# Performance work log

Hardware: AMD Instinct MI355X
Metric: run time of the kernel (lower is better)

The kernel has to match this reference:

```python
import jax, jax.numpy as jnp
import numpy as np

NUM_HEADS = 4
K_RATIO = 0.01
K_NEIGHBORS = 8
DIM = 256


def setup_inputs() -> dict:
    key = jax.random.key(0)
    ks = jax.random.split(key, 11)
    d, nh = DIM, NUM_HEADS
    def lin(k, out_f, in_f):
        return jax.random.normal(k, (out_f, in_f), jnp.float32) / np.sqrt(in_f)
    return {
        "x": jax.random.normal(ks[0], (32, d, 64, 64), jnp.float32),
        # graph_modulator: Conv2d(d, d//4, 1) -> ReLU -> Conv2d(d//4, nh, 1) -> Sigmoid
        "gm_w1": lin(ks[1], d // 4, d),
        "gm_b1": jnp.zeros((d // 4,), jnp.float32),
        "gm_w2": lin(ks[2], nh, d // 4),
        "gm_b2": jnp.zeros((nh,), jnp.float32),
        # local_qkv: Linear(d, 3d, bias=False)
        "qkv_w": lin(ks[3], 3 * d, d),
        # graph_encoder: Linear(d, d//2) -> ReLU -> Linear(d//2, nh)
        "ge_w1": lin(ks[4], d // 2, d),
        "ge_b1": jnp.zeros((d // 2,), jnp.float32),
        "ge_w2": lin(ks[5], nh, d // 2),
        "ge_b2": jnp.zeros((nh,), jnp.float32),
    }


def _forward(x, gm_w1, gm_b1, gm_w2, gm_b2, qkv_w, ge_w1, ge_b1, ge_w2, ge_b2):
    B, C, H, W = x.shape
    nh = NUM_HEADS
    hd = C // nh
    scale = hd ** -0.5
    HW = H * W

    # spatial modulation: two 1x1 convs
    h1 = jax.nn.relu(jnp.einsum("bchw,oc->bohw", x, gm_w1) + gm_b1[None, :, None, None])
    spatial_mod = jax.nn.sigmoid(jnp.einsum("bchw,oc->bohw", h1, gm_w2) + gm_b2[None, :, None, None])  # [B,nh,H,W]

    # top-k pixel selection by mean-abs importance
    num_select = min(max(1, int(HW * K_RATIO)), 64)  # static
    importance = jnp.mean(jnp.abs(x), axis=1).reshape(B, HW)
    _, top_idx = jax.lax.top_k(importance, num_select)  # [B,S]

    x_flat = x.reshape(B, C, HW).transpose(0, 2, 1)  # [B,HW,C]
    sel = jnp.take_along_axis(x_flat, top_idx[:, :, None], axis=1)  # [B,S,C]

    def per_batch(feat):  # feat: [S,C]
        S = feat.shape[0]
        # kNN graph on L2-normalized features (F.normalize eps=1e-12)
        n = jnp.maximum(jnp.linalg.norm(feat, axis=1, keepdims=True), 1e-12)
        nf = feat / n
        sim = nf @ nf.T  # [S,S]
        _, nbr = jax.lax.top_k(sim, K_NEIGHBORS + 1)  # [S,k+1]
        rows = jnp.arange(S)[:, None]
        mask = jnp.zeros((S, S), feat.dtype).at[rows, nbr].set(1.0)
        mask = mask * (1.0 - jnp.eye(S, dtype=feat.dtype))  # no self-loops
        # qkv
        qkv = (feat @ qkv_w.T).reshape(S, 3, nh, hd).transpose(1, 2, 0, 3)  # [3,nh,S,hd]
        q, k, v = qkv[0], qkv[1], qkv[2]
        scores = jnp.einsum("hsd,htd->hst", q, k) * scale  # [nh,S,S]
        # graph modulation (same for every head in the torch loop)
        gw = jax.nn.relu(feat @ ge_w1.T + ge_b1) @ ge_w2.T + ge_b2  # [S,nh]
        pair = (gw @ gw.T) / nh  # mean over heads of gw_src*gw_dst
        scores = scores + 0.1 * (mask * pair)[None]
        attn = jax.nn.softmax(scores, axis=-1)
        return attn.mean(axis=(0, 2))  # [S] pixel importance

    pixel_imp = jax.vmap(per_batch)(sel)  # [B,S]

    gmw_flat = jnp.zeros((B, HW), x.dtype).at[jnp.arange(B)[:, None], top_idx].set(pixel_imp)
    graph_mod = jnp.broadcast_to(gmw_flat.reshape(B, 1, H, W), (B, nh, H, W))

    final_mod = 0.7 * spatial_mod + 0.3 * graph_mod
    return x * jnp.mean(final_mod, axis=1, keepdims=True)


def reference(x, gm_w1, gm_b1, gm_w2, gm_b2, qkv_w, ge_w1, ge_b1, ge_w2, ge_b2):
    return _forward(x, gm_w1, gm_b1, gm_w2, gm_b2, qkv_w, ge_w1, ge_b1, ge_w2, ge_b2)
```

## Files before the change

kernel.cpp:

```cpp
#include <hip/hip_runtime.h>
#include <cfloat>

#define B_    32
#define C_    256
#define HW_   4096
#define NH_   4
#define HID_  64
#define SSEL_ 40
#define GADD_ 0.0075f

__global__ __launch_bounds__(256) void k_mlp(
    const float* __restrict__ x,
    const float* __restrict__ w1, const float* __restrict__ b1,
    const float* __restrict__ w2, const float* __restrict__ b2,
    float* __restrict__ m, float* __restrict__ imp)
{
    __shared__ float XT[32 * 128];
    __shared__ float WT[32 * 64];
    __shared__ float H1[64 * 128];
    __shared__ float SAB[256 * 4];

    const int t  = threadIdx.x;
    const int b  = blockIdx.x >> 5;
    const int p0 = (blockIdx.x & 31) * 128;
    const float* __restrict__ xb = x + ((size_t)b << 20) + p0;

    const int pxg  = t & 31;
    const int hidg = t >> 5;

    float acc[8][4];
    #pragma unroll
    for (int j = 0; j < 8; ++j) {
        const float bj = b1[hidg * 8 + j];
        #pragma unroll
        for (int p = 0; p < 4; ++p) acc[j][p] = bj;
    }
    float4 sa = make_float4(0.f, 0.f, 0.f, 0.f);

    for (int kk = 0; kk < 8; ++kk) {
        const int c0 = kk * 32;
        if (kk) __syncthreads();
        #pragma unroll
        for (int i = 0; i < 4; ++i) {
            const int q   = t + i * 256;
            const int row = q >> 5;
            const float4 v = *(const float4*)(xb + (size_t)(c0 + row) * HW_ + pxg * 4);
            *(float4*)(XT + row * 128 + pxg * 4) = v;
            sa.x += fabsf(v.x); sa.y += fabsf(v.y);
            sa.z += fabsf(v.z); sa.w += fabsf(v.w);
        }
        #pragma unroll
        for (int i = 0; i < 8; ++i) {
            const int q = t + i * 256;
            const int k = q >> 6, j = q & 63;
            WT[k * 64 + j] = w1[j * C_ + c0 + k];
        }
        __syncthreads();
        #pragma unroll
        for (int k = 0; k < 32; ++k) {
            const float4 xv = *(const float4*)(XT + k * 128 + pxg * 4);
            const float4 wa = *(const float4*)(WT + k * 64 + hidg * 8);
            const float4 wb = *(const float4*)(WT + k * 64 + hidg * 8 + 4);
            const float xr[4] = {xv.x, xv.y, xv.z, xv.w};
            const float wr[8] = {wa.x, wa.y, wa.z, wa.w, wb.x, wb.y, wb.z, wb.w};
            #pragma unroll
            for (int j = 0; j < 8; ++j)
                #pragma unroll
                for (int p = 0; p < 4; ++p)
                    acc[j][p] = fmaf(wr[j], xr[p], acc[j][p]);
        }
    }

    #pragma unroll
    for (int j = 0; j < 8; ++j) {
        float4 hv;
        hv.x = fmaxf(acc[j][0], 0.f);
        hv.y = fmaxf(acc[j][1], 0.f);
        hv.z = fmaxf(acc[j][2], 0.f);
        hv.w = fmaxf(acc[j][3], 0.f);
        *(float4*)(H1 + (hidg * 8 + j) * 128 + pxg * 4) = hv;
    }
    *(float4*)(SAB + t * 4) = sa;
    __syncthreads();

    if (t < 32) {
        float4 s = make_float4(0.f, 0.f, 0.f, 0.f);
        #pragma unroll
        for (int g = 0; g < 8; ++g) {
            const float4 v = *(const float4*)(SAB + (g * 32 + t) * 4);
            s.x += v.x; s.y += v.y; s.z += v.z; s.w += v.w;
        }
        *(float4*)(imp + ((size_t)b << 12) + p0 + t * 4) = s;
    }
    if (t < 128) {
        const int px = t;
        float s0 = b2[0], s1 = b2[1], s2 = b2[2], s3 = b2[3];
        #pragma unroll 8
        for (int j = 0; j < 64; ++j) {
            const float h = H1[j * 128 + px];
            s0 = fmaf(w2[0 * HID_ + j], h, s0);
            s1 = fmaf(w2[1 * HID_ + j], h, s1);
            s2 = fmaf(w2[2 * HID_ + j], h, s2);
            s3 = fmaf(w2[3 * HID_ + j], h, s3);
        }
        const float ssum = 1.f / (1.f + __expf(-s0)) + 1.f / (1.f + __expf(-s1))
                         + 1.f / (1.f + __expf(-s2)) + 1.f / (1.f + __expf(-s3));
        m[((size_t)b << 12) + p0 + px] = 0.175f * ssum;
    }
}

__global__ __launch_bounds__(64) void k_topk(
    const float* __restrict__ imp, float* __restrict__ m)
{
    const int b    = blockIdx.x;
    const int lane = threadIdx.x;
    const float* __restrict__ ib = imp + (size_t)b * HW_;
    float* __restrict__ mb = m + (size_t)b * HW_;

    float v[64];
    #pragma unroll
    for (int i = 0; i < 64; ++i) v[i] = ib[i * 64 + lane];

    float g[8];
    #pragma unroll
    for (int k = 0; k < 8; ++k) {
        float gm = v[8 * k];
        #pragma unroll
        for (int i = 1; i < 8; ++i) gm = fmaxf(gm, v[8 * k + i]);
        g[k] = gm;
    }

    for (int it = 0; it < SSEL_; ++it) {
        float lm = g[0];
        #pragma unroll
        for (int k = 1; k < 8; ++k) lm = fmaxf(lm, g[k]);
        float wm = lm;
        #pragma unroll
        for (int off = 32; off >= 1; off >>= 1)
            wm = fmaxf(wm, __shfl_xor(wm, off, 64));
        #pragma unroll
        for (int k = 0; k < 8; ++k) {
            if (__any(g[k] == wm)) {
                int gi = -1;
                #pragma unroll
                for (int i = 0; i < 8; ++i) {
                    if (v[8 * k + i] == wm) {
                        gi = (8 * k + i) * 64 + lane;
                        v[8 * k + i] = -FLT_MAX;
                    }
                }
                float gm = v[8 * k];
                #pragma unroll
                for (int i = 1; i < 8; ++i) gm = fmaxf(gm, v[8 * k + i]);
                g[k] = gm;
                if (gi >= 0) mb[gi] += GADD_;
            }
        }
    }
}

__global__ __launch_bounds__(256) void k_apply(
    const float4* __restrict__ x4, const float* __restrict__ m,
    float4* __restrict__ o4)
{
    const size_t i = (size_t)blockIdx.x * 256 + threadIdx.x;
    const size_t flat = i << 2;
    const int b = (int)(flat >> 20);
    const int p = (int)(flat & (HW_ - 1));
    const float4 mv = *(const float4*)(m + ((size_t)b << 12) + p);
    const float4 xv = x4[i];
    float4 r;
    r.x = xv.x * mv.x; r.y = xv.y * mv.y;
    r.z = xv.z * mv.z; r.w = xv.w * mv.w;
    o4[i] = r;
}

extern "C" void kernel_launch(void* const* d_in, const int* in_sizes, int n_in,
                              void* d_out, int out_size, void* d_ws, size_t ws_size,
                              hipStream_t stream)
{
    const float* x  = (const float*)d_in[0];
    const float* w1 = (const float*)d_in[1];
    const float* b1 = (const float*)d_in[2];
    const float* w2 = (const float*)d_in[3];
    const float* b2 = (const float*)d_in[4];

    float* m   = (float*)d_ws;
    float* imp = m + (size_t)B_ * HW_;
    float* out = (float*)d_out;

    k_mlp<<<dim3(B_ * (HW_ / 128)), dim3(256), 0, stream>>>(x, w1, b1, w2, b2, m, imp);
    k_topk<<<dim3(B_), dim3(64), 0, stream>>>(imp, m);
    const int n4 = (B_ * C_ * HW_) / 4;
    k_apply<<<dim3(n4 / 256), dim3(256), 0, stream>>>((const float4*)x, m, (float4*)out);
}
```

Measured before the change: 330.0 us.

## Compute first 1x1 conv with fp16 MFMA and swizzled LDS tiles

Replaces the scalar FP32 FMA GEMM for the hidden layer of the spatial modulator with fp16 MFMA 16x16x32 instructions. Weights and x tiles are converted to half and staged in XOR-swizzled shared memory. The block covers 256 pixels and each thread handles one pixel's abs-sum. The second conv is reduced via lane shuffles from the MFMA accumulators. This removes the compute-bound FP32 FMA loop, at the cost of fp16 rounding of x and weights, which could shift importance/modulation values slightly.

```diff
diff --git a/kernel.cpp b/kernel.cpp
--- a/kernel.cpp
+++ b/kernel.cpp
@@ -1,5 +1,6 @@
 #include <hip/hip_runtime.h>
 #include <cfloat>
+#include <cstdint>
 
 #define B_    32
 #define C_    256
@@ -9,103 +10,135 @@
 #define SSEL_ 40
 #define GADD_ 0.0075f
 
-__global__ __launch_bounds__(256) void k_mlp(
+using half8_t = __attribute__((ext_vector_type(8))) _Float16;
+using half4_t = __attribute__((ext_vector_type(4))) _Float16;
+using f32x4_t = __attribute__((ext_vector_type(4))) float;
+
+__global__ __launch_bounds__(256, 2) void k_mlp(
     const float* __restrict__ x,
     const float* __restrict__ w1, const float* __restrict__ b1,
     const float* __restrict__ w2, const float* __restrict__ b2,
     float* __restrict__ m, float* __restrict__ imp)
 {
-    __shared__ float XT[32 * 128];
-    __shared__ float WT[32 * 64];
-    __shared__ float H1[64 * 128];
-    __shared__ float SAB[256 * 4];
-
-    const int t  = threadIdx.x;
-    const int b  = blockIdx.x >> 5;
-    const int p0 = (blockIdx.x & 31) * 128;
-    const float* __restrict__ xb = x + ((size_t)b << 20) + p0;
-
-    const int pxg  = t & 31;
-    const int hidg = t >> 5;
-
-    float acc[8][4];
-    #pragma unroll
-    for (int j = 0; j < 8; ++j) {
-        const float bj = b1[hidg * 8 + j];
-        #pragma unroll
-        for (int p = 0; p < 4; ++p) acc[j][p] = bj;
-    }
-    float4 sa = make_float4(0.f, 0.f, 0.f, 0.f);
-
-    for (int kk = 0; kk < 8; ++kk) {
-        const int c0 = kk * 32;
-        if (kk) __syncthreads();
-        #pragma unroll
-        for (int i = 0; i < 4; ++i) {
-            const int q   = t + i * 256;
-            const int row = q >> 5;
-            const float4 v = *(const float4*)(xb + (size_t)(c0 + row) * HW_ + pxg * 4);
-            *(float4*)(XT + row * 128 + pxg * 4) = v;
-            sa.x += fabsf(v.x); sa.y += fabsf(v.y);
-            sa.z += fabsf(v.z); sa.w += fabsf(v.w);
-        }
-        #pragma unroll
-        for (int i = 0; i < 8; ++i) {
-            const int q = t + i * 256;
-            const int k = q >> 6, j = q & 63;
-            WT[k * 64 + j] = w1[j * C_ + c0 + k];
+    __shared__ __align__(16) uint32_t WHu[64 * 128];
+    __shared__ __align__(16) uint32_t XTu[256 * 32];
+
+    const int t    = threadIdx.x;
+    const int b    = blockIdx.x >> 4;
+    const int p0   = (blockIdx.x & 15) << 8;
+    const int lane = t & 63;
+    const int wv   = t >> 6;
+    const int g    = lane >> 4;
+    const int lr   = lane & 15;
+
+    #pragma unroll
+    for (int i = 0; i < 16; ++i) {
+        const int q   = t + (i << 8);
+        const int hid = q >> 6;
+        const float4 wq = *(const float4*)(w1 + ((size_t)q << 2));
+        half4_t hv;
+        hv[0] = (_Float16)wq.x; hv[1] = (_Float16)wq.y;
+        hv[2] = (_Float16)wq.z; hv[3] = (_Float16)wq.w;
+        const int col = ((q & 63) * 2) ^ ((hid & 7) << 2);
+        *reinterpret_cast<half4_t*>(&WHu[hid * 128 + col]) = hv;
+    }
+
+    f32x4_t acc[4][4];
+    #pragma unroll
+    for (int mt = 0; mt < 4; ++mt) {
+        const float4 bv = *(const float4*)(b1 + mt * 16 + g * 4);
+        #pragma unroll
+        for (int nt = 0; nt < 4; ++nt) {
+            acc[mt][nt][0] = bv.x; acc[mt][nt][1] = bv.y;
+            acc[mt][nt][2] = bv.z; acc[mt][nt][3] = bv.w;
+        }
+    }
+
+    float sa = 0.f;
+    const float* __restrict__ xb = x + ((size_t)b << 20) + p0 + t;
+
+    for (int ck = 0; ck < 4; ++ck) {
+        if (ck) __syncthreads();
+        const float* __restrict__ xc = xb + ((size_t)(ck * 64) << 12);
+        #pragma unroll
+        for (int jo = 0; jo < 8; ++jo) {
+            float v[8];
+            #pragma unroll
+            for (int e = 0; e < 8; ++e) v[e] = xc[(size_t)(jo * 8 + e) << 12];
+            half8_t hv;
+            #pragma unroll
+            for (int e = 0; e < 8; ++e) {
+                hv[e] = (_Float16)v[e];
+                sa += fabsf(v[e]);
+            }
+            const int col = (jo * 4) ^ ((t & 7) << 2);
+            *reinterpret_cast<half8_t*>(&XTu[t * 32 + col]) = hv;
         }
         __syncthreads();
         #pragma unroll
-        for (int k = 0; k < 32; ++k) {
-            const float4 xv = *(const float4*)(XT + k * 128 + pxg * 4);
-            const float4 wa = *(const float4*)(WT + k * 64 + hidg * 8);
-            const float4 wb = *(const float4*)(WT + k * 64 + hidg * 8 + 4);
-            const float xr[4] = {xv.x, xv.y, xv.z, xv.w};
-            const float wr[8] = {wa.x, wa.y, wa.z, wa.w, wb.x, wb.y, wb.z, wb.w};
-            #pragma unroll
-            for (int j = 0; j < 8; ++j)
+        for (int k2 = 0; k2 < 2; ++k2) {
+            const int ks = ck * 2 + k2;
+            half8_t af[4], bf[4];
+            #pragma unroll
+            for (int mt = 0; mt < 4; ++mt) {
+                const int hid = mt * 16 + lr;
+                const int col = (ks * 16 + g * 4) ^ ((hid & 7) << 2);
+                af[mt] = *reinterpret_cast<const half8_t*>(&WHu[hid * 128 + col]);
+            }
+            #pragma unroll
+            for (int nt = 0; nt < 4; ++nt) {
+                const int px = wv * 64 + nt * 16 + lr;
+                const int col = (k2 * 16 + g * 4) ^ ((px & 7) << 2);
+                bf[nt] = *reinterpret_cast<const half8_t*>(&XTu[px * 32 + col]);
+            }
+            #pragma unroll
+            for (int mt = 0; mt < 4; ++mt)
                 #pragma unroll
-                for (int p = 0; p < 4; ++p)
-                    acc[j][p] = fmaf(wr[j], xr[p], acc[j][p]);
-        }
-    }
-
-    #pragma unroll
-    for (int j = 0; j < 8; ++j) {
-        float4 hv;
-        hv.x = fmaxf(acc[j][0], 0.f);
-        hv.y = fmaxf(acc[j][1], 0.f);
-        hv.z = fmaxf(acc[j][2], 0.f);
-        hv.w = fmaxf(acc[j][3], 0.f);
-        *(float4*)(H1 + (hidg * 8 + j) * 128 + pxg * 4) = hv;
-    }
-    *(float4*)(SAB + t * 4) = sa;
-    __syncthreads();
-
-    if (t < 32) {
-        float4 s = make_float4(0.f, 0.f, 0.f, 0.f);
-        #pragma unroll
-        for (int g = 0; g < 8; ++g) {
-            const float4 v = *(const float4*)(SAB + (g * 32 + t) * 4);
-            s.x += v.x; s.y += v.y; s.z += v.z; s.w += v.w;
-        }
-        *(float4*)(imp + ((size_t)b << 12) + p0 + t * 4) = s;
-    }
-    if (t < 128) {
-        const int px = t;
-        float s0 = b2[0], s1 = b2[1], s2 = b2[2], s3 = b2[3];
-        #pragma unroll 8
-        for (int j = 0; j < 64; ++j) {
-            const float h = H1[j * 128 + px];
-            s0 = fmaf(w2[0 * HID_ + j], h, s0);
-            s1 = fmaf(w2[1 * HID_ + j], h, s1);
-            s2 = fmaf(w2[2 * HID_ + j], h, s2);
-            s3 = fmaf(w2[3 * HID_ + j], h, s3);
-        }
-        const float ssum = 1.f / (1.f + __expf(-s0)) + 1.f / (1.f + __expf(-s1))
-                         + 1.f / (1.f + __expf(-s2)) + 1.f / (1.f + __expf(-s3));
-        m[((size_t)b << 12) + p0 + px] = 0.175f * ssum;
+                for (int nt = 0; nt < 4; ++nt)
+                    acc[mt][nt] = __builtin_amdgcn_mfma_f32_16x16x32_f16(
+                        af[mt], bf[nt], acc[mt][nt], 0, 0, 0);
+        }
+    }
+
+    imp[((size_t)b << 12) + p0 + t] = sa;
+
+    float4 w2r[4][4];
+    #pragma unroll
+    for (int hd = 0; hd < 4; ++hd)
+        #pragma unroll
+        for (int mt = 0; mt < 4; ++mt)
+            w2r[hd][mt] = *(const float4*)(w2 + hd * 64 + mt * 16 + g * 4);
+
+    #pragma unroll
+    for (int nt = 0; nt < 4; ++nt) {
+        float s[4] = {0.f, 0.f, 0.f, 0.f};
+        #pragma unroll
+        for (int mt = 0; mt < 4; ++mt) {
+            const float h0 = fmaxf(acc[mt][nt][0], 0.f);
+            const float h1 = fmaxf(acc[mt][nt][1], 0.f);
+            const float h2 = fmaxf(acc[mt][nt][2], 0.f);
+            const float h3 = fmaxf(acc[mt][nt][3], 0.f);
+            #pragma unroll
+            for (int hd = 0; hd < 4; ++hd) {
+                s[hd] = fmaf(w2r[hd][mt].x, h0, s[hd]);
+                s[hd] = fmaf(w2r[hd][mt].y, h1, s[hd]);
+                s[hd] = fmaf(w2r[hd][mt].z, h2, s[hd]);
+                s[hd] = fmaf(w2r[hd][mt].w, h3, s[hd]);
+            }
+        }
+        #pragma unroll
+        for (int hd = 0; hd < 4; ++hd) {
+            s[hd] += __shfl_xor(s[hd], 16, 64);
+            s[hd] += __shfl_xor(s[hd], 32, 64);
+        }
+        if (g == 0) {
+            const float ssum =
+                  1.f / (1.f + __expf(-(s[0] + b2[0])))
+                + 1.f / (1.f + __expf(-(s[1] + b2[1])))
+                + 1.f / (1.f + __expf(-(s[2] + b2[2])))
+                + 1.f / (1.f + __expf(-(s[3] + b2[3])));
+            m[((size_t)b << 12) + p0 + wv * 64 + nt * 16 + lr] = 0.175f * ssum;
+        }
     }
 }
 
@@ -189,7 +222,7 @@
     float* imp = m + (size_t)B_ * HW_;
     float* out = (float*)d_out;
 
-    k_mlp<<<dim3(B_ * (HW_ / 128)), dim3(256), 0, stream>>>(x, w1, b1, w2, b2, m, imp);
+    k_mlp<<<dim3(B_ * (HW_ / 256)), dim3(256), 0, stream>>>(x, w1, b1, w2, b2, m, imp);
     k_topk<<<dim3(B_), dim3(64), 0, stream>>>(imp, m);
     const int n4 = (B_ * C_ * HW_) / 4;
     k_apply<<<dim3(n4 / 256), dim3(256), 0, stream>>>((const float4*)x, m, (float4*)out);
```

New measurement: 293.6 us. 11.0% less time.
